# Performance work log

Hardware: AMD Instinct MI355X
Metric: run time of the kernel (lower is better)

The kernel has to match this reference:

```python
import jax, jax.numpy as jnp
import numpy as np

TEMP = 0.1
COEFF = 0.5
WARMUP = 0
S = 32 * 32  # hardcoded in the torch module


def _l2n(x, axis):
    # matches F.normalize(p=2, eps=1e-12)
    n = jnp.linalg.norm(x, axis=axis, keepdims=True)
    return x / jnp.maximum(n, 1e-12)


def _ce_first_class(pos, neg):
    # cross-entropy with label 0 on logits = [pos | neg] / T
    logits = jnp.concatenate([pos, neg], axis=1) / TEMP
    return jnp.mean(jax.nn.logsumexp(logits, axis=1) - logits[:, 0])


def _dense_losses(q_of, q_x, k_of, k_x, k_avg_dense):
    # q_of,k_of: (B,d,S) normalized; q_x,k_x: (B,C,S) normalized; k_avg_dense: (B,C) UN-normalized (torch bug preserved)
    B, C, _ = q_x.shape
    sim = jnp.einsum('bds,bdt->bst', q_of, k_of)          # (B,S,S)
    ind = jnp.argmax(sim, axis=2)                          # (B,S)
    idxg = jnp.take_along_axis(k_x, jnp.broadcast_to(ind[:, None, :], k_x.shape), axis=2)
    idxg = jax.lax.stop_gradient(idxg)                     # computed under torch.no_grad
    l_pos = jnp.sum(q_x * idxg, axis=1).reshape(-1, 1)     # (B*S,1)
    qf = jnp.transpose(q_x, (0, 2, 1)).reshape(-1, C)      # (B*S,C)
    l_neg_full = qf @ k_avg_dense.T                        # (B*S,B)
    # static mask: row n excludes column n // S
    base = np.stack([np.delete(np.arange(B), i) for i in range(B)])  # (B,B-1)
    neg_cols = jnp.asarray(np.repeat(base, S, axis=0))     # (B*S,B-1)
    l_neg = jnp.take_along_axis(l_neg_full, neg_cols, axis=1)
    return l_pos, l_neg


def _forward(original_features_q, avgpooled_global_q, x_q, avgpooled_dense_q,
             original_features_k, avgpooled_global_k, x_k, avgpooled_dense_k, epoch):
    of = jnp.concatenate([original_features_q, original_features_k], axis=0)
    ag = jnp.concatenate([avgpooled_global_q, avgpooled_global_k], axis=0)
    x = jnp.concatenate([x_q, x_k], axis=0)
    ad = jnp.concatenate([avgpooled_dense_q, avgpooled_dense_k], axis=0)

    # global InfoNCE
    agn = _l2n(ag, 1)
    sim = agn @ agn.T                                      # (2B,2B)
    n2 = sim.shape[0]
    B = n2 // 2
    rows = np.arange(n2)
    pos_cols = (rows + B) % n2
    pos = sim[jnp.asarray(rows), jnp.asarray(pos_cols)][:, None]
    neg_cols = np.stack([np.setdiff1d(rows, [i, pos_cols[i]]) for i in range(n2)])  # (2B,2B-2)
    neg = jnp.take_along_axis(sim, jnp.asarray(neg_cols), axis=1)
    global_loss = _ce_first_class(pos, neg)

    # dense InfoNCE
    b, d, h, w = of.shape
    of = _l2n(of.reshape(b, d, h * w), 1)
    xn = _l2n(x, 1)
    q_of, k_of = of[:b // 2], of[b // 2:]
    q_x, k_x = xn[:b // 2], xn[b // 2:]
    q_ad, k_ad = ad[:b // 2], ad[b // 2:]  # NOTE: un-normalized, matching the torch code
    p1, n1 = _dense_losses(q_of, q_x, k_of, k_x, k_ad)
    p2, n2_ = _dense_losses(k_of, k_x, q_of, q_x, q_ad)
    dense_loss = _ce_first_class(jnp.concatenate([p1, p2], axis=0),
                                 jnp.concatenate([n1, n2_], axis=0))

    if epoch > WARMUP:
        return COEFF * global_loss + (1.0 - COEFF) * dense_loss
    return global_loss


def setup_inputs() -> dict:
    key = jax.random.key(0)
    ks = jax.random.split(key, 8)
    B, d, C, h, w = 64, 256, 128, 32, 32
    return {
        'original_features_q': jax.random.normal(ks[0], (B, d, h, w), jnp.float32),
        'avgpooled_global_q': jax.random.normal(ks[1], (B, C), jnp.float32),
        'x_q': jax.random.normal(ks[2], (B, C, h * w), jnp.float32),
        'avgpooled_dense_q': jax.random.normal(ks[3], (B, C), jnp.float32),
        'original_features_k': jax.random.normal(ks[4], (B, d, h, w), jnp.float32),
        'avgpooled_global_k': jax.random.normal(ks[5], (B, C), jnp.float32),
        'x_k': jax.random.normal(ks[6], (B, C, h * w), jnp.float32),
        'avgpooled_dense_k': jax.random.normal(ks[7], (B, C), jnp.float32),
        'epoch': 5,
    }


def reference(original_features_q, avgpooled_global_q, x_q, avgpooled_dense_q,
              original_features_k, avgpooled_global_k, x_k, avgpooled_dense_k, epoch):
    return _forward(original_features_q, avgpooled_global_q, x_q, avgpooled_dense_q,
                    original_features_k, avgpooled_global_k, x_k, avgpooled_dense_k, epoch)
```

## Files before the change

kernel.cpp:

```cpp
#include <hip/hip_runtime.h>
#include <math.h>

#define TEMP_INV 10.0f

typedef unsigned long long u64;
typedef __attribute__((ext_vector_type(8))) __bf16 bf16x8;
typedef __attribute__((ext_vector_type(4))) float f32x4;

__device__ inline u64 packmax(float v, unsigned int idx) {
  unsigned int u = __float_as_uint(v);
  unsigned int key = (u & 0x80000000u) ? ~u : (u | 0x80000000u);
  return ((u64)key << 32) | (u64)(0xFFFFFFFFu - idx);
}

__device__ __forceinline__ void async_copy16(const void* gp, void* lp) {
  __builtin_amdgcn_global_load_lds(
      (__attribute__((address_space(1))) void*)(unsigned long long)gp,
      (__attribute__((address_space(3))) void*)(unsigned long long)lp,
      16, 0, 0);
}

__global__ __launch_bounds__(256) void kcvt(const float* __restrict__ ofq,
                                            const float* __restrict__ ofk,
                                            __bf16* __restrict__ ofT,
                                            float* __restrict__ of_invn) {
  int s0 = blockIdx.x * 32, b = blockIdx.y;
  const float* src = (b < 64) ? (ofq + (size_t)b * 262144) : (ofk + (size_t)(b - 64) * 262144);
  __shared__ __bf16 T[32][36];
  __shared__ float R[8][32];
  int t = threadIdx.x;
  int dd = t >> 5, ss = t & 31;
  int wr = t >> 3, wd = t & 7;
  float ssq = 0.f;
  __bf16* out = ofT + (size_t)b * 262144 + (size_t)s0 * 256;
  for (int d0 = 0; d0 < 256; d0 += 32) {
    float v[4];
#pragma unroll
    for (int it = 0; it < 4; ++it) {
      int d = d0 + dd + 8 * it;
      v[it] = src[(size_t)d * 1024 + s0 + ss];
      ssq += v[it] * v[it];
    }
    __syncthreads();
#pragma unroll
    for (int it = 0; it < 4; ++it) T[ss][dd + 8 * it] = (__bf16)v[it];
    __syncthreads();
    *(uint2*)(out + (size_t)wr * 256 + d0 + wd * 4) = *(const uint2*)(&T[wr][wd * 4]);
  }
  R[dd][ss] = ssq;
  __syncthreads();
  if (t < 32) {
    float a = 0.f;
#pragma unroll
    for (int r = 0; r < 8; ++r) a += R[r][t];
    of_invn[b * 1024 + s0 + t] = 1.0f / fmaxf(sqrtf(a), 1e-12f);
  }
}

__global__ void knorm_x(const float* __restrict__ xq, const float* __restrict__ xk,
                        float* __restrict__ x_invn) {
  int idx = blockIdx.x * blockDim.x + threadIdx.x;
  int b = idx >> 10, s = idx & 1023;
  const float* src = (b < 64) ? (xq + (size_t)b * 131072) : (xk + (size_t)(b - 64) * 131072);
  float acc = 0.f;
#pragma unroll 8
  for (int c = 0; c < 128; ++c) { float v = src[c * 1024 + s]; acc += v * v; }
  x_invn[idx] = 1.0f / fmaxf(sqrtf(acc), 1e-12f);
}

__global__ void knorm_ag(const float* __restrict__ agq, const float* __restrict__ agk,
                         float* __restrict__ ag_invn) {
  int i = threadIdx.x;
  const float* row = (i < 64) ? (agq + i * 128) : (agk + (i - 64) * 128);
  float acc = 0.f;
#pragma unroll 8
  for (int c = 0; c < 128; ++c) { float v = row[c]; acc += v * v; }
  ag_invn[i] = 1.0f / fmaxf(sqrtf(acc), 1e-12f);
}

__global__ void ktrans_ad(const float* __restrict__ adq, const float* __restrict__ adk,
                          float* __restrict__ adt) {
  int i = blockIdx.x * 256 + threadIdx.x;
  int dir = i >> 13, r = i & 8191;
  int j = r >> 7, c = r & 127;
  const float* ad = dir == 0 ? adk : adq;
  adt[dir * 8192 + c * 64 + j] = ad[j * 128 + c];
}

__global__ __launch_bounds__(256) void ksim(
    const __bf16* __restrict__ ofT, const float* __restrict__ of_invn,
    u64* __restrict__ best_row, u64* __restrict__ best_col) {
  int b = blockIdx.z;
  int s0 = blockIdx.x * 128, t0 = blockIdx.y * 128;
  const __bf16* Ag = ofT + (size_t)b * 262144;
  const __bf16* Bg = ofT + (size_t)(b + 64) * 262144;
  __shared__ __bf16 As[4096];
  __shared__ __bf16 Bs[4096];
  __shared__ float siq[128], sik[128];
  int t = threadIdx.x;
  if (t < 128) siq[t] = of_invn[b * 1024 + s0 + t];
  else sik[t - 128] = of_invn[65536 + b * 1024 + t0 + (t - 128)];

  f32x4 acc[4][4];
#pragma unroll
  for (int i = 0; i < 4; ++i)
#pragma unroll
    for (int j = 0; j < 4; ++j) acc[i][j] = (f32x4)(0.f);

  int lane = t & 63, w = t >> 6;
  int lc = lane & 15, q = lane >> 4;
  int wm = w & 1, wn = w >> 1;

  int aoff[4], boff[4];
#pragma unroll
  for (int i = 0; i < 4; ++i) {
    int mr = wm * 64 + i * 16 + lc;
    aoff[i] = mr * 32 + (((q + mr + (mr >> 2)) & 3) << 3);
    int nc = wn * 64 + i * 16 + lc;
    boff[i] = nc * 32 + (((q + nc + (nc >> 2)) & 3) << 3);
  }

  int kp = t & 3;
  for (int k0 = 0; k0 < 256; k0 += 32) {
    __syncthreads();
#pragma unroll
    for (int r = 0; r < 2; ++r) {
      int m = r * 64 + (t >> 2);
      int lg = (kp - m - (m >> 2)) & 3;
      async_copy16(Ag + (size_t)(s0 + m) * 256 + k0 + lg * 8,
                   (char*)As + r * 4096 + t * 16);
      async_copy16(Bg + (size_t)(t0 + m) * 256 + k0 + lg * 8,
                   (char*)Bs + r * 4096 + t * 16);
    }
    __syncthreads();
    bf16x8 af[4], bfr[4];
#pragma unroll
    for (int i = 0; i < 4; ++i) af[i] = *(const bf16x8*)(As + aoff[i]);
#pragma unroll
    for (int j = 0; j < 4; ++j) bfr[j] = *(const bf16x8*)(Bs + boff[j]);
#pragma unroll
    for (int i = 0; i < 4; ++i)
#pragma unroll
      for (int j = 0; j < 4; ++j)
        acc[i][j] = __builtin_amdgcn_mfma_f32_16x16x32_bf16(af[i], bfr[j], acc[i][j], 0, 0, 0);
  }

  u64* browb = best_row + (size_t)b * 1024 + s0;
  u64* bcolb = best_col + (size_t)b * 1024 + t0;
#pragma unroll
  for (int i = 0; i < 4; ++i) {
    int rowq = wm * 64 + i * 16 + q * 4;
#pragma unroll
    for (int e = 0; e < 4; ++e) {
      u64 p = 0;
#pragma unroll
      for (int j = 0; j < 4; ++j) {
        int col = wn * 64 + j * 16 + lc;
        u64 pk = packmax(acc[i][j][e] * sik[col], (unsigned)(t0 + col));
        p = p > pk ? p : pk;
      }
#pragma unroll
      for (int mask = 1; mask <= 8; mask <<= 1) {
        u64 o = __shfl_xor(p, mask);
        p = p > o ? p : o;
      }
      if (lc == 0) atomicMax(browb + rowq + e, p);
    }
  }
#pragma unroll
  for (int j = 0; j < 4; ++j) {
    u64 p = 0;
#pragma unroll
    for (int i = 0; i < 4; ++i)
#pragma unroll
      for (int e = 0; e < 4; ++e) {
        int row = wm * 64 + i * 16 + q * 4 + e;
        u64 pk = packmax(acc[i][j][e] * siq[row], (unsigned)(s0 + row));
        p = p > pk ? p : pk;
      }
    u64 o = __shfl_xor(p, 16); p = p > o ? p : o;
    o = __shfl_xor(p, 32); p = p > o ? p : o;
    if (lane < 16) atomicMax(bcolb + wn * 64 + j * 16 + lane, p);
  }
}

__global__ __launch_bounds__(512) void kpos(
    const float* __restrict__ xq, const float* __restrict__ xk,
    const float* __restrict__ x_invn,
    const u64* __restrict__ best_row, const u64* __restrict__ best_col,
    float* __restrict__ posl) {
  int b = blockIdx.x, dir = blockIdx.y, sh = blockIdx.z;
  const float* xsrc = dir == 0 ? xq : xk;
  const float* xdst = dir == 0 ? xk : xq;
  const float* inv_src = x_invn + (dir ? 65536 : 0);
  const float* inv_dst = x_invn + (dir ? 0 : 65536);
  const u64* best = dir == 0 ? best_row : best_col;

  __shared__ float xrow[8][1024];
  __shared__ float sdinv[1024];
  int t = threadIdx.x;
  sdinv[t] = inv_dst[b * 1024 + t];
  sdinv[t + 512] = inv_dst[b * 1024 + t + 512];
  int s = sh * 512 + t;
  u64 p = best[(size_t)b * 1024 + s];
  int sidx = (int)(0xFFFFFFFFu - (unsigned)(p & 0xFFFFFFFFull));
  const float* xsb = xsrc + (size_t)b * 131072;
  const float* xdb = xdst + (size_t)b * 131072;
  float acc = 0.f;
  for (int c0 = 0; c0 < 128; c0 += 8) {
    __syncthreads();
#pragma unroll
    for (int qq = 0; qq < 4; ++qq)
      ((float4*)xrow)[t + 512 * qq] = ((const float4*)(xdb + (size_t)c0 * 1024))[t + 512 * qq];
    __syncthreads();
#pragma unroll
    for (int cc = 0; cc < 8; ++cc)
      acc += xsb[(size_t)(c0 + cc) * 1024 + s] * xrow[cc][sidx];
  }
  posl[dir * 65536 + b * 1024 + s] = acc * inv_src[b * 1024 + s] * sdinv[sidx] * TEMP_INV;
}

__global__ __launch_bounds__(256) void kneg(
    const float* __restrict__ xq, const float* __restrict__ xk,
    const float* __restrict__ x_invn,
    const float* __restrict__ adt, const float* __restrict__ posl,
    float* __restrict__ dsum) {
  int st = blockIdx.x, b = blockIdx.y, dir = blockIdx.z;
  const float* xsrc = dir == 0 ? xq : xk;
  const float* inv_src = x_invn + (dir ? 65536 : 0);
  const float* Bt = adt + dir * 8192;

  __shared__ float As2[64][64];
  __shared__ float Bs2[128][64];
  __shared__ float red[16];

  int tid = threadIdx.x;
  int tx = tid & 15, ty = tid >> 4;
  int s0 = st * 64;

#pragma unroll
  for (int qq = 0; qq < 8; ++qq)
    reinterpret_cast<float4*>(Bs2)[tid + 256 * qq] =
        reinterpret_cast<const float4*>(Bt)[tid + 256 * qq];

  float acc[4][4];
#pragma unroll
  for (int i = 0; i < 4; ++i)
#pragma unroll
    for (int j = 0; j < 4; ++j) acc[i][j] = 0.f;

  int lm = tid & 63, lk = tid >> 6;
  float sinv = inv_src[b * 1024 + s0 + lm];
  const float* xb = xsrc + (size_t)b * 131072;

  for (int k0 = 0; k0 < 128; k0 += 64) {
#pragma unroll
    for (int r = 0; r < 16; ++r) {
      int kk = lk + 4 * r;
      As2[kk][lm] = xb[(k0 + kk) * 1024 + s0 + lm] * sinv;
    }
    __syncthreads();
#pragma unroll
    for (int kk = 0; kk < 64; ++kk) {
      float4 av = *reinterpret_cast<const float4*>(&As2[kk][ty * 4]);
      float4 bv = *reinterpret_cast<const float4*>(&Bs2[k0 + kk][tx * 4]);
      float a[4] = {av.x, av.y, av.z, av.w};
      float bb[4] = {bv.x, bv.y, bv.z, bv.w};
#pragma unroll
      for (int i = 0; i < 4; ++i)
#pragma unroll
        for (int j = 0; j < 4; ++j) acc[i][j] += a[i] * bb[j];
    }
    __syncthreads();
  }

  float lsum = 0.f;
#pragma unroll
  for (int i = 0; i < 4; ++i) {
    int s = s0 + ty * 4 + i;
    float pos = posl[dir * 65536 + b * 1024 + s];
    float lg[4];
    float mloc = -INFINITY;
#pragma unroll
    for (int j = 0; j < 4; ++j) {
      int jg = tx * 4 + j;
      lg[j] = (jg == b) ? -INFINITY : acc[i][j] * TEMP_INV;
      mloc = fmaxf(mloc, lg[j]);
    }
#pragma unroll
    for (int mask = 1; mask <= 8; mask <<= 1) mloc = fmaxf(mloc, __shfl_xor(mloc, mask));
    float m = fmaxf(mloc, pos);
    float e = 0.f;
#pragma unroll
    for (int j = 0; j < 4; ++j) e += __expf(lg[j] - m);
#pragma unroll
    for (int mask = 1; mask <= 8; mask <<= 1) e += __shfl_xor(e, mask);
    if (tx == 0) lsum += m + __logf(e + __expf(pos - m)) - pos;
  }
  if (tx == 0) red[ty] = lsum;
  __syncthreads();
  if (tid == 0) {
    float v = 0.f;
#pragma unroll
    for (int r = 0; r < 16; ++r) v += red[r];
    atomicAdd(dsum, v);
  }
}

__global__ void kglobal(const float* __restrict__ agq, const float* __restrict__ agk,
                        const float* __restrict__ ag_invn, float* __restrict__ gsum) {
  __shared__ float logits[128];
  int i = blockIdx.x, j = threadIdx.x;
  const float* rowi = (i < 64) ? (agq + i * 128) : (agk + (i - 64) * 128);
  const float* rowj = (j < 64) ? (agq + j * 128) : (agk + (j - 64) * 128);
  float dot = 0.f;
#pragma unroll 8
  for (int c = 0; c < 128; ++c) dot += rowi[c] * rowj[c];
  logits[j] = dot * ag_invn[i] * ag_invn[j] * TEMP_INV;
  __syncthreads();
  if (j == 0) {
    int pos = (i + 64) & 127;
    float m = -INFINITY;
    for (int t = 0; t < 128; ++t) if (t != i) m = fmaxf(m, logits[t]);
    float e = 0.f;
    for (int t = 0; t < 128; ++t) if (t != i) e += __expf(logits[t] - m);
    atomicAdd(gsum, m + __logf(e) - logits[pos]);
  }
}

__global__ void kfinal(const float* __restrict__ gsum, const float* __restrict__ dsum,
                       const int* __restrict__ epoch, float* __restrict__ out) {
  if (threadIdx.x == 0) {
    float g = gsum[0] / 128.0f;
    float dn = dsum[0] / 131072.0f;
    out[0] = (epoch[0] > 0) ? (0.5f * g + 0.5f * dn) : g;
  }
}

extern "C" void kernel_launch(void* const* d_in, const int* in_sizes, int n_in,
                              void* d_out, int out_size, void* d_ws, size_t ws_size,
                              hipStream_t stream) {
  const float* ofq = (const float*)d_in[0];
  const float* agq = (const float*)d_in[1];
  const float* xq  = (const float*)d_in[2];
  const float* adq = (const float*)d_in[3];
  const float* ofk = (const float*)d_in[4];
  const float* agk = (const float*)d_in[5];
  const float* xk  = (const float*)d_in[6];
  const float* adk = (const float*)d_in[7];
  const int* epoch = (const int*)d_in[8];
  float* out = (float*)d_out;

  char* wsb = (char*)d_ws;
  __bf16* ofT = (__bf16*)wsb;
  u64* best_row = (u64*)(wsb + 67108864);
  u64* best_col = best_row + 65536;
  float* gsum = (float*)(best_col + 65536);
  float* dsum = gsum + 1;
  float* posl = dsum + 1;
  float* of_invn = posl + 131072;
  float* x_invn  = of_invn + 131072;
  float* ag_invn = x_invn + 131072;
  float* adt = ag_invn + 128;

  hipMemsetAsync(best_row, 0, 65536ull * 8 * 2 + 8, stream);

  dim3 gc(32, 128);
  kcvt<<<gc, 256, 0, stream>>>(ofq, ofk, ofT, of_invn);
  knorm_x<<<512, 256, 0, stream>>>(xq, xk, x_invn);
  knorm_ag<<<1, 128, 0, stream>>>(agq, agk, ag_invn);
  ktrans_ad<<<64, 256, 0, stream>>>(adq, adk, adt);

  dim3 gs(8, 8, 64);
  ksim<<<gs, 256, 0, stream>>>(ofT, of_invn, best_row, best_col);

  dim3 gp(64, 2, 2);
  kpos<<<gp, 512, 0, stream>>>(xq, xk, x_invn, best_row, best_col, posl);

  dim3 gn(16, 64, 2);
  kneg<<<gn, 256, 0, stream>>>(xq, xk, x_invn, adt, posl, dsum);

  kglobal<<<128, 128, 0, stream>>>(agq, agk, ag_invn, gsum);
  kfinal<<<1, 1, 0, stream>>>(gsum, dsum, epoch, out);
}
```

Measured before the change: 424.9 us.

## Double-buffer ksim loads, split argmax reductions, and fuse small prep kernels

ksim now double-buffers its LDS tiles so the async global-to-LDS copies for the next k-slice overlap with the MFMAs on the current one, with one barrier per iteration instead of two. The argmax epilogue reduces 32-bit float maxima first and then the index, replacing 64-bit packed shuffles. knorm_x and ktrans_ad are merged into one kprep launch, and the ag norm is folded into kglobal, which removes launches. kpos uses 1024-thread blocks instead of two 512-thread halves. This doubles ksim's LDS use and gives kpos a larger block, which may lower occupancy.

```diff
diff --git a/kernel.cpp b/kernel.cpp
--- a/kernel.cpp
+++ b/kernel.cpp
@@ -7,10 +7,12 @@
 typedef __attribute__((ext_vector_type(8))) __bf16 bf16x8;
 typedef __attribute__((ext_vector_type(4))) float f32x4;
 
-__device__ inline u64 packmax(float v, unsigned int idx) {
-  unsigned int u = __float_as_uint(v);
-  unsigned int key = (u & 0x80000000u) ? ~u : (u | 0x80000000u);
-  return ((u64)key << 32) | (u64)(0xFFFFFFFFu - idx);
+__device__ inline unsigned fkey(float v) {
+  unsigned u = __float_as_uint(v);
+  return (u & 0x80000000u) ? ~u : (u | 0x80000000u);
+}
+__device__ inline u64 packvi(float v, unsigned idx) {
+  return ((u64)fkey(v) << 32) | (u64)(0xFFFFFFFFu - idx);
 }
 
 __device__ __forceinline__ void async_copy16(const void* gp, void* lp) {
@@ -57,34 +59,25 @@
   }
 }
 
-__global__ void knorm_x(const float* __restrict__ xq, const float* __restrict__ xk,
-                        float* __restrict__ x_invn) {
-  int idx = blockIdx.x * blockDim.x + threadIdx.x;
-  int b = idx >> 10, s = idx & 1023;
-  const float* src = (b < 64) ? (xq + (size_t)b * 131072) : (xk + (size_t)(b - 64) * 131072);
-  float acc = 0.f;
+__global__ void kprep(const float* __restrict__ xq, const float* __restrict__ xk,
+                      float* __restrict__ x_invn,
+                      const float* __restrict__ adq, const float* __restrict__ adk,
+                      float* __restrict__ adt) {
+  if (blockIdx.x < 512) {
+    int idx = blockIdx.x * 256 + threadIdx.x;
+    int b = idx >> 10, s = idx & 1023;
+    const float* src = (b < 64) ? (xq + (size_t)b * 131072) : (xk + (size_t)(b - 64) * 131072);
+    float acc = 0.f;
 #pragma unroll 8
-  for (int c = 0; c < 128; ++c) { float v = src[c * 1024 + s]; acc += v * v; }
-  x_invn[idx] = 1.0f / fmaxf(sqrtf(acc), 1e-12f);
-}
-
-__global__ void knorm_ag(const float* __restrict__ agq, const float* __restrict__ agk,
-                         float* __restrict__ ag_invn) {
-  int i = threadIdx.x;
-  const float* row = (i < 64) ? (agq + i * 128) : (agk + (i - 64) * 128);
-  float acc = 0.f;
-#pragma unroll 8
-  for (int c = 0; c < 128; ++c) { float v = row[c]; acc += v * v; }
-  ag_invn[i] = 1.0f / fmaxf(sqrtf(acc), 1e-12f);
-}
-
-__global__ void ktrans_ad(const float* __restrict__ adq, const float* __restrict__ adk,
-                          float* __restrict__ adt) {
-  int i = blockIdx.x * 256 + threadIdx.x;
-  int dir = i >> 13, r = i & 8191;
-  int j = r >> 7, c = r & 127;
-  const float* ad = dir == 0 ? adk : adq;
-  adt[dir * 8192 + c * 64 + j] = ad[j * 128 + c];
+    for (int c = 0; c < 128; ++c) { float v = src[c * 1024 + s]; acc += v * v; }
+    x_invn[idx] = 1.0f / fmaxf(sqrtf(acc), 1e-12f);
+  } else {
+    int i = (blockIdx.x - 512) * 256 + threadIdx.x;
+    int dir = i >> 13, r = i & 8191;
+    int j = r >> 7, c = r & 127;
+    const float* ad = dir == 0 ? adk : adq;
+    adt[dir * 8192 + c * 64 + j] = ad[j * 128 + c];
+  }
 }
 
 __global__ __launch_bounds__(256) void ksim(
@@ -94,8 +87,8 @@
   int s0 = blockIdx.x * 128, t0 = blockIdx.y * 128;
   const __bf16* Ag = ofT + (size_t)b * 262144;
   const __bf16* Bg = ofT + (size_t)(b + 64) * 262144;
-  __shared__ __bf16 As[4096];
-  __shared__ __bf16 Bs[4096];
+  __shared__ __bf16 As[2][4096];
+  __shared__ __bf16 Bs[2][4096];
   __shared__ float siq[128], sik[128];
   int t = threadIdx.x;
   if (t < 128) siq[t] = of_invn[b * 1024 + s0 + t];
@@ -121,75 +114,102 @@
   }
 
   int kp = t & 3;
-  for (int k0 = 0; k0 < 256; k0 += 32) {
-    __syncthreads();
-#pragma unroll
-    for (int r = 0; r < 2; ++r) {
-      int m = r * 64 + (t >> 2);
-      int lg = (kp - m - (m >> 2)) & 3;
-      async_copy16(Ag + (size_t)(s0 + m) * 256 + k0 + lg * 8,
-                   (char*)As + r * 4096 + t * 16);
-      async_copy16(Bg + (size_t)(t0 + m) * 256 + k0 + lg * 8,
-                   (char*)Bs + r * 4096 + t * 16);
-    }
-    __syncthreads();
+  int mA0 = t >> 2, lgA0 = (kp - mA0 - (mA0 >> 2)) & 3;
+  int mA1 = 64 + (t >> 2), lgA1 = (kp - mA1 - (mA1 >> 2)) & 3;
+
+  async_copy16(Ag + (size_t)(s0 + mA0) * 256 + lgA0 * 8, (char*)&As[0][0] + t * 16);
+  async_copy16(Bg + (size_t)(t0 + mA0) * 256 + lgA0 * 8, (char*)&Bs[0][0] + t * 16);
+  async_copy16(Ag + (size_t)(s0 + mA1) * 256 + lgA1 * 8, (char*)&As[0][0] + 4096 + t * 16);
+  async_copy16(Bg + (size_t)(t0 + mA1) * 256 + lgA1 * 8, (char*)&Bs[0][0] + 4096 + t * 16);
+  __syncthreads();
+
+  for (int it = 0; it < 8; ++it) {
+    int buf = it & 1;
     bf16x8 af[4], bfr[4];
 #pragma unroll
-    for (int i = 0; i < 4; ++i) af[i] = *(const bf16x8*)(As + aoff[i]);
-#pragma unroll
-    for (int j = 0; j < 4; ++j) bfr[j] = *(const bf16x8*)(Bs + boff[j]);
+    for (int i = 0; i < 4; ++i) af[i] = *(const bf16x8*)(&As[buf][0] + aoff[i]);
+#pragma unroll
+    for (int j = 0; j < 4; ++j) bfr[j] = *(const bf16x8*)(&Bs[buf][0] + boff[j]);
+    if (it < 7) {
+      int k0 = (it + 1) * 32;
+      async_copy16(Ag + (size_t)(s0 + mA0) * 256 + k0 + lgA0 * 8, (char*)&As[buf ^ 1][0] + t * 16);
+      async_copy16(Bg + (size_t)(t0 + mA0) * 256 + k0 + lgA0 * 8, (char*)&Bs[buf ^ 1][0] + t * 16);
+      async_copy16(Ag + (size_t)(s0 + mA1) * 256 + k0 + lgA1 * 8, (char*)&As[buf ^ 1][0] + 4096 + t * 16);
+      async_copy16(Bg + (size_t)(t0 + mA1) * 256 + k0 + lgA1 * 8, (char*)&Bs[buf ^ 1][0] + 4096 + t * 16);
+    }
 #pragma unroll
     for (int i = 0; i < 4; ++i)
 #pragma unroll
       for (int j = 0; j < 4; ++j)
         acc[i][j] = __builtin_amdgcn_mfma_f32_16x16x32_bf16(af[i], bfr[j], acc[i][j], 0, 0, 0);
-  }
+    __syncthreads();
+  }
+
+  float sk[4], sq[16];
+#pragma unroll
+  for (int j = 0; j < 4; ++j) sk[j] = sik[wn * 64 + j * 16 + lc];
+#pragma unroll
+  for (int i = 0; i < 4; ++i)
+#pragma unroll
+    for (int e = 0; e < 4; ++e) sq[i * 4 + e] = siq[wm * 64 + i * 16 + q * 4 + e];
 
   u64* browb = best_row + (size_t)b * 1024 + s0;
   u64* bcolb = best_col + (size_t)b * 1024 + t0;
+
 #pragma unroll
   for (int i = 0; i < 4; ++i) {
-    int rowq = wm * 64 + i * 16 + q * 4;
 #pragma unroll
     for (int e = 0; e < 4; ++e) {
-      u64 p = 0;
+      float v[4];
+#pragma unroll
+      for (int j = 0; j < 4; ++j) v[j] = acc[i][j][e] * sk[j];
+      float vb = fmaxf(fmaxf(v[0], v[1]), fmaxf(v[2], v[3]));
+#pragma unroll
+      for (int mask = 1; mask <= 8; mask <<= 1) vb = fmaxf(vb, __shfl_xor(vb, mask));
+      unsigned ib = 0xFFFFFFFFu;
 #pragma unroll
       for (int j = 0; j < 4; ++j) {
-        int col = wn * 64 + j * 16 + lc;
-        u64 pk = packmax(acc[i][j][e] * sik[col], (unsigned)(t0 + col));
-        p = p > pk ? p : pk;
+        unsigned cand = (v[j] == vb) ? (unsigned)(t0 + wn * 64 + j * 16 + lc) : 0xFFFFFFFFu;
+        ib = min(ib, cand);
       }
 #pragma unroll
-      for (int mask = 1; mask <= 8; mask <<= 1) {
-        u64 o = __shfl_xor(p, mask);
-        p = p > o ? p : o;
+      for (int mask = 1; mask <= 8; mask <<= 1) ib = min(ib, __shfl_xor(ib, mask));
+      if (lc == 0)
+        atomicMax(browb + wm * 64 + i * 16 + q * 4 + e, ((u64)fkey(vb) << 32) | (u64)(0xFFFFFFFFu - ib));
+    }
+  }
+
+#pragma unroll
+  for (int j = 0; j < 4; ++j) {
+    float cb = -INFINITY;
+#pragma unroll
+    for (int i = 0; i < 4; ++i)
+#pragma unroll
+      for (int e = 0; e < 4; ++e) cb = fmaxf(cb, acc[i][j][e] * sq[i * 4 + e]);
+    cb = fmaxf(cb, __shfl_xor(cb, 16));
+    cb = fmaxf(cb, __shfl_xor(cb, 32));
+    unsigned ib = 0xFFFFFFFFu;
+#pragma unroll
+    for (int i = 0; i < 4; ++i)
+#pragma unroll
+      for (int e = 0; e < 4; ++e) {
+        float m2 = acc[i][j][e] * sq[i * 4 + e];
+        unsigned cand = (m2 == cb) ? (unsigned)(s0 + wm * 64 + i * 16 + q * 4 + e) : 0xFFFFFFFFu;
+        ib = min(ib, cand);
       }
-      if (lc == 0) atomicMax(browb + rowq + e, p);
-    }
-  }
-#pragma unroll
-  for (int j = 0; j < 4; ++j) {
-    u64 p = 0;
-#pragma unroll
-    for (int i = 0; i < 4; ++i)
-#pragma unroll
-      for (int e = 0; e < 4; ++e) {
-        int row = wm * 64 + i * 16 + q * 4 + e;
-        u64 pk = packmax(acc[i][j][e] * siq[row], (unsigned)(s0 + row));
-        p = p > pk ? p : pk;
-      }
-    u64 o = __shfl_xor(p, 16); p = p > o ? p : o;
-    o = __shfl_xor(p, 32); p = p > o ? p : o;
-    if (lane < 16) atomicMax(bcolb + wn * 64 + j * 16 + lane, p);
-  }
-}
-
-__global__ __launch_bounds__(512) void kpos(
+    ib = min(ib, __shfl_xor(ib, 16));
+    ib = min(ib, __shfl_xor(ib, 32));
+    if (lane < 16)
+      atomicMax(bcolb + wn * 64 + j * 16 + lane, ((u64)fkey(cb) << 32) | (u64)(0xFFFFFFFFu - ib));
+  }
+}
+
+__global__ __launch_bounds__(1024) void kpos(
     const float* __restrict__ xq, const float* __restrict__ xk,
     const float* __restrict__ x_invn,
     const u64* __restrict__ best_row, const u64* __restrict__ best_col,
     float* __restrict__ posl) {
-  int b = blockIdx.x, dir = blockIdx.y, sh = blockIdx.z;
+  int b = blockIdx.x, dir = blockIdx.y;
   const float* xsrc = dir == 0 ? xq : xk;
   const float* xdst = dir == 0 ? xk : xq;
   const float* inv_src = x_invn + (dir ? 65536 : 0);
@@ -200,9 +220,7 @@
   __shared__ float sdinv[1024];
   int t = threadIdx.x;
   sdinv[t] = inv_dst[b * 1024 + t];
-  sdinv[t + 512] = inv_dst[b * 1024 + t + 512];
-  int s = sh * 512 + t;
-  u64 p = best[(size_t)b * 1024 + s];
+  u64 p = best[(size_t)b * 1024 + t];
   int sidx = (int)(0xFFFFFFFFu - (unsigned)(p & 0xFFFFFFFFull));
   const float* xsb = xsrc + (size_t)b * 131072;
   const float* xdb = xdst + (size_t)b * 131072;
@@ -210,14 +228,14 @@
   for (int c0 = 0; c0 < 128; c0 += 8) {
     __syncthreads();
 #pragma unroll
-    for (int qq = 0; qq < 4; ++qq)
-      ((float4*)xrow)[t + 512 * qq] = ((const float4*)(xdb + (size_t)c0 * 1024))[t + 512 * qq];
+    for (int qq = 0; qq < 2; ++qq)
+      ((float4*)xrow)[t + 1024 * qq] = ((const float4*)(xdb + (size_t)c0 * 1024))[t + 1024 * qq];
     __syncthreads();
 #pragma unroll
     for (int cc = 0; cc < 8; ++cc)
-      acc += xsb[(size_t)(c0 + cc) * 1024 + s] * xrow[cc][sidx];
-  }
-  posl[dir * 65536 + b * 1024 + s] = acc * inv_src[b * 1024 + s] * sdinv[sidx] * TEMP_INV;
+      acc += xsb[(size_t)(c0 + cc) * 1024 + t] * xrow[cc][sidx];
+  }
+  posl[dir * 65536 + b * 1024 + t] = acc * inv_src[b * 1024 + t] * sdinv[sidx] * TEMP_INV;
 }
 
 __global__ __launch_bounds__(256) void kneg(
@@ -308,15 +326,18 @@
 }
 
 __global__ void kglobal(const float* __restrict__ agq, const float* __restrict__ agk,
-                        const float* __restrict__ ag_invn, float* __restrict__ gsum) {
+                        float* __restrict__ gsum) {
   __shared__ float logits[128];
+  __shared__ float rinv[128];
   int i = blockIdx.x, j = threadIdx.x;
   const float* rowi = (i < 64) ? (agq + i * 128) : (agk + (i - 64) * 128);
   const float* rowj = (j < 64) ? (agq + j * 128) : (agk + (j - 64) * 128);
-  float dot = 0.f;
+  float dot = 0.f, nj = 0.f;
 #pragma unroll 8
-  for (int c = 0; c < 128; ++c) dot += rowi[c] * rowj[c];
-  logits[j] = dot * ag_invn[i] * ag_invn[j] * TEMP_INV;
+  for (int c = 0; c < 128; ++c) { float a = rowi[c], bb = rowj[c]; dot += a * bb; nj += bb * bb; }
+  rinv[j] = 1.0f / fmaxf(sqrtf(nj), 1e-12f);
+  __syncthreads();
+  logits[j] = dot * rinv[i] * rinv[j] * TEMP_INV;
   __syncthreads();
   if (j == 0) {
     int pos = (i + 64) & 127;
@@ -358,28 +379,25 @@
   float* gsum = (float*)(best_col + 65536);
   float* dsum = gsum + 1;
   float* posl = dsum + 1;
-  float* of_invn = posl + 131072;
-  float* x_invn  = of_invn + 131072;
-  float* ag_invn = x_invn + 131072;
-  float* adt = ag_invn + 128;
+  float* x_invn  = posl + 131072;
+  float* of_invn = x_invn + 131072;
+  float* adt = of_invn + 131072;
 
   hipMemsetAsync(best_row, 0, 65536ull * 8 * 2 + 8, stream);
 
   dim3 gc(32, 128);
   kcvt<<<gc, 256, 0, stream>>>(ofq, ofk, ofT, of_invn);
-  knorm_x<<<512, 256, 0, stream>>>(xq, xk, x_invn);
-  knorm_ag<<<1, 128, 0, stream>>>(agq, agk, ag_invn);
-  ktrans_ad<<<64, 256, 0, stream>>>(adq, adk, adt);
+  kprep<<<576, 256, 0, stream>>>(xq, xk, x_invn, adq, adk, adt);
+  kglobal<<<128, 128, 0, stream>>>(agq, agk, gsum);
 
   dim3 gs(8, 8, 64);
   ksim<<<gs, 256, 0, stream>>>(ofT, of_invn, best_row, best_col);
 
-  dim3 gp(64, 2, 2);
-  kpos<<<gp, 512, 0, stream>>>(xq, xk, x_invn, best_row, best_col, posl);
+  dim3 gp(64, 2);
+  kpos<<<gp, 1024, 0, stream>>>(xq, xk, x_invn, best_row, best_col, posl);
 
   dim3 gn(16, 64, 2);
   kneg<<<gn, 256, 0, stream>>>(xq, xk, x_invn, adt, posl, dsum);
 
-  kglobal<<<128, 128, 0, stream>>>(agq, agk, ag_invn, gsum);
   kfinal<<<1, 1, 0, stream>>>(gsum, dsum, epoch, out);
 }
```

Result: no change. 422.4 us (-0.6%).
